# Performance work log

Hardware: AMD Instinct MI355X
Metric: run time of the kernel (lower is better)

## Reference

```python
import jax, jax.numpy as jnp
import numpy as np

DIM = 768
NUM_HEADS = 8
HEAD_DIM = DIM // NUM_HEADS


def setup_inputs() -> dict:
    key = jax.random.key(0)
    k1, k2, k3, k4, k5 = jax.random.split(key, 5)
    B, C, H, W = 16, DIM, 32, 32
    x = jax.random.normal(k1, (B, C, H, W), dtype=jnp.float32)
    # Conv2d 1x1 weights expressed as [out_ch, in_ch] matrices
    w_qkv = jax.random.normal(k2, (3 * C, C), dtype=jnp.float32) * (C ** -0.5)
    b_qkv = jax.random.normal(k3, (3 * C,), dtype=jnp.float32) * 0.02
    w_proj = jax.random.normal(k4, (C, C), dtype=jnp.float32) * (C ** -0.5)
    b_proj = jax.random.normal(k5, (C,), dtype=jnp.float32) * 0.02
    return {"x": x, "w_qkv": w_qkv, "b_qkv": b_qkv, "w_proj": w_proj, "b_proj": b_proj}


def reference(x, w_qkv, b_qkv, w_proj, b_proj):
    B, C, H, W = x.shape
    N = H * W
    nh, hd = NUM_HEADS, C // NUM_HEADS
    xf = x.astype(jnp.float32).reshape(B, C, N)  # bcn
    # 1x1 conv == channel matmul
    qkv = jnp.einsum('oc,bcn->bon', w_qkv, xf) + b_qkv[None, :, None]
    qkv = qkv.reshape(B, 3, nh, hd, N)
    q, k, v = qkv[:, 0], qkv[:, 1], qkv[:, 2]  # [B, nh, hd, N]
    s = hd ** -0.25  # scale split between q and k as in the original
    attn = jnp.einsum('bhdn,bhdm->bhnm', q * s, k * s)  # [B, nh, N, N]
    attn = attn - jax.lax.stop_gradient(jnp.max(attn, axis=-1, keepdims=True))
    attn = jnp.clip(attn, -88.0, 88.0)
    attn = jax.nn.softmax(attn, axis=-1)
    # dropout is identity in eval mode
    out = jnp.einsum('bhnm,bhdm->bhdn', attn, v)  # [B, nh, hd, N]
    out = out.reshape(B, C, N)
    out = jnp.einsum('oc,bcn->bon', w_proj, out) + b_proj[None, :, None]
    return out.reshape(B, C, H, W).astype(x.dtype)
```

## Files before the change

### kernel.cpp

```cpp
#include <hip/hip_runtime.h>
#include <stdint.h>

typedef __attribute__((ext_vector_type(4))) float f32x4;
typedef __attribute__((ext_vector_type(16))) float f32x16;
typedef __attribute__((ext_vector_type(8))) short bf16x8;

#define SQKV 0.38372606f

__device__ __forceinline__ unsigned short f2bf(float f) {
  union { float f; unsigned u; } v; v.f = f;
  unsigned r = v.u + 0x7FFFu + ((v.u >> 16) & 1u);
  return (unsigned short)(r >> 16);
}

__device__ __forceinline__ unsigned cvt_pk_bf16(float a, float b) {
  unsigned r;
  asm volatile("v_cvt_pk_bf16_f32 %0, %1, %2" : "=v"(r) : "v"(a), "v"(b));
  return r;
}
__device__ __forceinline__ void permswap(unsigned &a, unsigned &b) {
  asm volatile("v_permlane32_swap_b32 %0, %1" : "+v"(a), "+v"(b));
}

__device__ __forceinline__ void glds16(const unsigned short* g, unsigned short* l) {
  __builtin_amdgcn_global_load_lds(
      (const __attribute__((address_space(1))) void*)g,
      (__attribute__((address_space(3))) void*)l, 16, 0, 0);
}

__global__ __launch_bounds__(256) void k_convert(const float* __restrict__ src,
                                                 unsigned short* __restrict__ dst,
                                                 int n4) {
  int i = blockIdx.x * 256 + threadIdx.x;
  if (i >= n4) return;
  float4 v = reinterpret_cast<const float4*>(src)[i];
  ushort4 o;
  o.x = f2bf(v.x); o.y = f2bf(v.y); o.z = f2bf(v.z); o.w = f2bf(v.w);
  reinterpret_cast<ushort4*>(dst)[i] = o;
}

__global__ __launch_bounds__(256) void k_transpose(const float* __restrict__ x,
                                                   unsigned short* __restrict__ xT) {
  __shared__ float tile[32][33];
  const int t = threadIdx.x;
  const int j = t & 31, i0 = t >> 5;
  const int n0 = blockIdx.x * 32, c0 = blockIdx.y * 32, b = blockIdx.z;
  const float* src = x + ((size_t)b * 768 + c0) * 1024 + n0;
#pragma unroll
  for (int q = 0; q < 4; ++q)
    tile[i0 + q * 8][j] = src[(size_t)(i0 + q * 8) * 1024 + j];
  __syncthreads();
  unsigned short* dst = xT + ((size_t)b * 1024 + n0) * 768 + c0;
#pragma unroll
  for (int q = 0; q < 4; ++q)
    dst[(size_t)(i0 + q * 8) * 768 + j] = f2bf(tile[j][i0 + q * 8]);
}

__global__ __launch_bounds__(256, 4) void k_gemm_qkv(
    const unsigned short* __restrict__ A,
    const unsigned short* __restrict__ Bx,
    const float* __restrict__ bias,
    unsigned short* __restrict__ qT,
    unsigned short* __restrict__ kT,
    unsigned short* __restrict__ vO) {
  __shared__ unsigned short As[128 * 32];
  __shared__ unsigned short Bs[128 * 32];
  const int t = threadIdx.x;
  const int b = blockIdx.y;
  const int tm = blockIdx.x >> 3, tn = blockIdx.x & 7;
  const int lane = t & 63, w = t >> 6, wr = w >> 1, wc = w & 1;

  const int srow = 16 * w + (lane >> 2);
  const int scol = (lane & 3) << 3;
  const unsigned short* aptr0 = A + (size_t)(tm * 128 + srow) * 768 + scol;
  const unsigned short* aptr1 = aptr0 + (size_t)64 * 768;
  const unsigned short* bptr0 = Bx + (size_t)b * 1024 * 768 + (size_t)(tn * 128 + srow) * 768 + scol;
  const unsigned short* bptr1 = bptr0 + (size_t)64 * 768;
  unsigned short* const lA0 = As + 512 * w;
  unsigned short* const lA1 = As + 2048 + 512 * w;
  unsigned short* const lB0 = Bs + 512 * w;
  unsigned short* const lB1 = Bs + 2048 + 512 * w;

  f32x4 acc[4][4];
#pragma unroll
  for (int mi = 0; mi < 4; ++mi)
#pragma unroll
    for (int ni = 0; ni < 4; ++ni) acc[mi][ni] = (f32x4)0.0f;

  const unsigned short* rA[4];
  const unsigned short* rB[4];
#pragma unroll
  for (int mi = 0; mi < 4; ++mi)
    rA[mi] = As + (wr * 64 + mi * 16 + (lane & 15)) * 32 + ((lane >> 4) << 3);
#pragma unroll
  for (int ni = 0; ni < 4; ++ni)
    rB[ni] = Bs + (wc * 64 + ni * 16 + (lane & 15)) * 32 + ((lane >> 4) << 3);

  for (int kt = 0; kt < 24; ++kt) {
    __syncthreads();
    glds16(aptr0, lA0);
    glds16(aptr1, lA1);
    glds16(bptr0, lB0);
    glds16(bptr1, lB1);
    aptr0 += 32; aptr1 += 32; bptr0 += 32; bptr1 += 32;
    __syncthreads();

    bf16x8 af[4], bfr[4];
#pragma unroll
    for (int mi = 0; mi < 4; ++mi) af[mi] = *reinterpret_cast<const bf16x8*>(rA[mi]);
#pragma unroll
    for (int ni = 0; ni < 4; ++ni) bfr[ni] = *reinterpret_cast<const bf16x8*>(rB[ni]);
#pragma unroll
    for (int mi = 0; mi < 4; ++mi)
#pragma unroll
      for (int ni = 0; ni < 4; ++ni)
        acc[mi][ni] = __builtin_amdgcn_mfma_f32_16x16x32_bf16(af[mi], bfr[ni], acc[mi][ni], 0, 0, 0);
  }

#pragma unroll
  for (int mi = 0; mi < 4; ++mi) {
    const int o0 = tm * 128 + wr * 64 + mi * 16 + ((lane >> 4) << 2);
    const float4 bb = *reinterpret_cast<const float4*>(bias + o0);
    const float sc = (o0 < 1536) ? SQKV : 1.0f;
    const int om = o0 % 768;
    const int hh = om / 96;
    const int d0 = om % 96;
    const int region = o0 / 768;
    const size_t bh = (size_t)(b * 8 + hh);
#pragma unroll
    for (int ni = 0; ni < 4; ++ni) {
      const int nn = tn * 128 + wc * 64 + ni * 16 + (lane & 15);
      ushort4 st;
      st.x = f2bf((acc[mi][ni][0] + bb.x) * sc);
      st.y = f2bf((acc[mi][ni][1] + bb.y) * sc);
      st.z = f2bf((acc[mi][ni][2] + bb.z) * sc);
      st.w = f2bf((acc[mi][ni][3] + bb.w) * sc);
      if (region == 0) {
        *reinterpret_cast<ushort4*>(qT + (bh * 1024 + nn) * 96 + d0) = st;
      } else if (region == 1) {
        *reinterpret_cast<ushort4*>(kT + (bh * 1024 + nn) * 96 + d0) = st;
      } else {
        unsigned short* vp = vO + (bh * 96 + d0) * 1024 + nn;
        vp[0] = st.x; vp[1024] = st.y; vp[2048] = st.z; vp[3072] = st.w;
      }
    }
  }
}

__global__ __launch_bounds__(512, 2) void k_attn2(
    const unsigned short* __restrict__ qT,
    const unsigned short* __restrict__ kT,
    const unsigned short* __restrict__ vO,
    unsigned short* __restrict__ attoutT) {
  __shared__ unsigned short Ks[2][64 * 104];
  __shared__ unsigned short Vs[2][96 * 72];
  __shared__ float redbuf[8][32];

  const int t = threadIdx.x, lane = t & 63, wv = t >> 6;
  const int r31 = lane & 31, h = lane >> 5;
  const int sw = (blockIdx.x & 7) * 64 + (blockIdx.x >> 3);
  const int bh = sw >> 2, qt = sw & 3;
  const int b = bh >> 3, hh = bh & 7;
  const int n0 = qt * 256 + wv * 32;

  bf16x8 Qf[6];
  {
    const unsigned short* qrow = qT + ((size_t)bh * 1024 + n0 + r31) * 96 + h * 8;
#pragma unroll
    for (int ks = 0; ks < 6; ++ks)
      Qf[ks] = *reinterpret_cast<const bf16x8*>(qrow + ks * 16);
  }

  const unsigned short* gptr[3];
  unsigned short* lptr[3];
  int gstep[3], lstride[3];
#pragma unroll
  for (int i = 0; i < 3; ++i) {
    const int cc = t + i * 512;
    if (cc < 768) {
      const int row = cc / 12, col = (cc % 12) * 8;
      gptr[i] = kT + ((size_t)bh * 1024 + row) * 96 + col;
      lptr[i] = &Ks[0][row * 104 + col];
      gstep[i] = 64 * 96;
      lstride[i] = 64 * 104;
    } else {
      const int cv = cc - 768;
      const int d = cv >> 3, col = (cv & 7) * 8;
      gptr[i] = vO + ((size_t)bh * 96 + d) * 1024 + col;
      lptr[i] = &Vs[0][d * 72 + col];
      gstep[i] = 64;
      lstride[i] = 96 * 72;
    }
  }
  uint4 rg[3];
#pragma unroll
  for (int i = 0; i < 3; ++i) rg[i] = *reinterpret_cast<const uint4*>(gptr[i]);

  f32x16 oac[3];
#pragma unroll
  for (int dt = 0; dt < 3; ++dt) oac[dt] = (f32x16)0.0f;
  float run_m = -3.0e38f, run_l = 0.0f;

  int cur = 0;
  for (int mt = 0; mt < 16; ++mt, cur ^= 1) {
#pragma unroll
    for (int i = 0; i < 3; ++i)
      *reinterpret_cast<uint4*>(lptr[i] + cur * lstride[i]) = rg[i];
    __syncthreads();
    if (mt < 15) {
#pragma unroll
      for (int i = 0; i < 3; ++i) {
        gptr[i] += gstep[i];
        rg[i] = *reinterpret_cast<const uint4*>(gptr[i]);
      }
    }
    const unsigned short* Kb = &Ks[cur][0];
    const unsigned short* Vb = &Vs[cur][0];

    f32x16 sa = (f32x16)0.0f, sb = (f32x16)0.0f;
    __builtin_amdgcn_s_setprio(1);
#pragma unroll
    for (int ks = 0; ks < 6; ++ks) {
      const bf16x8 k0 = *reinterpret_cast<const bf16x8*>(Kb + r31 * 104 + ks * 16 + h * 8);
      const bf16x8 k1 = *reinterpret_cast<const bf16x8*>(Kb + (32 + r31) * 104 + ks * 16 + h * 8);
      sa = __builtin_amdgcn_mfma_f32_32x32x16_bf16(k0, Qf[ks], sa, 0, 0, 0);
      sb = __builtin_amdgcn_mfma_f32_32x32x16_bf16(k1, Qf[ks], sb, 0, 0, 0);
    }
    __builtin_amdgcn_s_setprio(0);

    float m4a = fmaxf(sa[0], sa[1]), m4b = fmaxf(sa[2], sa[3]);
    float m4c = fmaxf(sb[0], sb[1]), m4d = fmaxf(sb[2], sb[3]);
#pragma unroll
    for (int i = 4; i < 16; i += 4) {
      m4a = fmaxf(m4a, fmaxf(sa[i], sa[i + 1]));
      m4b = fmaxf(m4b, fmaxf(sa[i + 2], sa[i + 3]));
      m4c = fmaxf(m4c, fmaxf(sb[i], sb[i + 1]));
      m4d = fmaxf(m4d, fmaxf(sb[i + 2], sb[i + 3]));
    }
    float tmax = fmaxf(fmaxf(m4a, m4b), fmaxf(m4c, m4d));
    tmax = fmaxf(tmax, __shfl_xor(tmax, 32));

    if (__any(tmax - run_m > 8.0f)) {
      const float nm = fmaxf(run_m, tmax);
      const float alpha = __builtin_amdgcn_exp2f(run_m - nm);
      run_m = nm;
      run_l *= alpha;
      if (lane < 32) redbuf[wv][lane] = alpha;
      f32x4 a4[4];
#pragma unroll
      for (int q = 0; q < 4; ++q)
        a4[q] = *reinterpret_cast<const f32x4*>(&redbuf[wv][q * 8 + h * 4]);
#pragma unroll
      for (int dt = 0; dt < 3; ++dt)
#pragma unroll
        for (int q = 0; q < 4; ++q)
#pragma unroll
          for (int j = 0; j < 4; ++j)
            oac[dt][q * 4 + j] *= a4[q][j];
    }

    float t0 = 0.f, t1 = 0.f, t2 = 0.f, t3 = 0.f;
#pragma unroll
    for (int i = 0; i < 16; i += 4) {
      sa[i]     = __builtin_amdgcn_exp2f(sa[i] - run_m);     t0 += sa[i];
      sa[i + 1] = __builtin_amdgcn_exp2f(sa[i + 1] - run_m); t1 += sa[i + 1];
      sa[i + 2] = __builtin_amdgcn_exp2f(sa[i + 2] - run_m); t2 += sa[i + 2];
      sa[i + 3] = __builtin_amdgcn_exp2f(sa[i + 3] - run_m); t3 += sa[i + 3];
    }
#pragma unroll
    for (int i = 0; i < 16; i += 4) {
      sb[i]     = __builtin_amdgcn_exp2f(sb[i] - run_m);     t0 += sb[i];
      sb[i + 1] = __builtin_amdgcn_exp2f(sb[i + 1] - run_m); t1 += sb[i + 1];
      sb[i + 2] = __builtin_amdgcn_exp2f(sb[i + 2] - run_m); t2 += sb[i + 2];
      sb[i + 3] = __builtin_amdgcn_exp2f(sb[i + 3] - run_m); t3 += sb[i + 3];
    }
    float ts = (t0 + t1) + (t2 + t3);
    ts += __shfl_xor(ts, 32);
    run_l += ts;

    union { bf16x8 v; unsigned u[4]; } pf;
    __builtin_amdgcn_s_setprio(1);
#pragma unroll
    for (int kst = 0; kst < 4; ++kst) {
      const f32x16& s = (kst < 2) ? sa : sb;
      const int base = (kst & 1) * 8;
      unsigned X = cvt_pk_bf16(s[base + 0], s[base + 1]);
      unsigned Y = cvt_pk_bf16(s[base + 2], s[base + 3]);
      unsigned Z = cvt_pk_bf16(s[base + 4], s[base + 5]);
      unsigned W = cvt_pk_bf16(s[base + 6], s[base + 7]);
      permswap(X, Z);
      permswap(Y, W);
      pf.u[0] = X; pf.u[1] = Y; pf.u[2] = Z; pf.u[3] = W;
#pragma unroll
      for (int dt = 0; dt < 3; ++dt) {
        const bf16x8 vf = *reinterpret_cast<const bf16x8*>(
            Vb + (dt * 32 + r31) * 72 + kst * 16 + h * 8);
        oac[dt] = __builtin_amdgcn_mfma_f32_32x32x16_bf16(pf.v, vf, oac[dt], 0, 0, 0);
      }
    }
    __builtin_amdgcn_s_setprio(0);
  }

  if (lane < 32) redbuf[wv][lane] = 1.0f / run_l;
  f32x4 i4[4];
#pragma unroll
  for (int q = 0; q < 4; ++q)
    i4[q] = *reinterpret_cast<const f32x4*>(&redbuf[wv][q * 8 + h * 4]);
  unsigned short* obase = attoutT + ((size_t)b * 1024 + n0) * 768 + hh * 96;
#pragma unroll
  for (int dt = 0; dt < 3; ++dt)
#pragma unroll
    for (int q = 0; q < 4; ++q)
#pragma unroll
      for (int j = 0; j < 4; ++j) {
        const int np = q * 8 + h * 4 + j;
        obase[(size_t)np * 768 + dt * 32 + r31] = f2bf(oac[dt][q * 4 + j] * i4[q][j]);
      }
}

__global__ __launch_bounds__(256, 4) void k_gemm_proj(
    const unsigned short* __restrict__ Aat,
    const unsigned short* __restrict__ Bw,
    const float* __restrict__ bias,
    float* __restrict__ out) {
  __shared__ unsigned short As[128 * 32];
  __shared__ unsigned short Bs[128 * 32];
  const int t = threadIdx.x;
  const int b = blockIdx.y;
  const int tm = blockIdx.x / 6, tn = blockIdx.x % 6;
  const int lane = t & 63, w = t >> 6, wr = w >> 1, wc = w & 1;

  const int srow = 16 * w + (lane >> 2);
  const int scol = (lane & 3) << 3;
  const unsigned short* aptr0 = Aat + (size_t)b * 1024 * 768 + (size_t)(tm * 128 + srow) * 768 + scol;
  const unsigned short* aptr1 = aptr0 + (size_t)64 * 768;
  const unsigned short* bptr0 = Bw + (size_t)(tn * 128 + srow) * 768 + scol;
  const unsigned short* bptr1 = bptr0 + (size_t)64 * 768;
  unsigned short* const lA0 = As + 512 * w;
  unsigned short* const lA1 = As + 2048 + 512 * w;
  unsigned short* const lB0 = Bs + 512 * w;
  unsigned short* const lB1 = Bs + 2048 + 512 * w;

  f32x4 acc[4][4];
#pragma unroll
  for (int mi = 0; mi < 4; ++mi)
#pragma unroll
    for (int ni = 0; ni < 4; ++ni) acc[mi][ni] = (f32x4)0.0f;

  const unsigned short* rA[4];
  const unsigned short* rB[4];
#pragma unroll
  for (int mi = 0; mi < 4; ++mi)
    rA[mi] = As + (wr * 64 + mi * 16 + (lane & 15)) * 32 + ((lane >> 4) << 3);
#pragma unroll
  for (int ni = 0; ni < 4; ++ni)
    rB[ni] = Bs + (wc * 64 + ni * 16 + (lane & 15)) * 32 + ((lane >> 4) << 3);

  for (int kt = 0; kt < 24; ++kt) {
    __syncthreads();
    glds16(aptr0, lA0);
    glds16(aptr1, lA1);
    glds16(bptr0, lB0);
    glds16(bptr1, lB1);
    aptr0 += 32; aptr1 += 32; bptr0 += 32; bptr1 += 32;
    __syncthreads();

    bf16x8 af[4], bfr[4];
#pragma unroll
    for (int mi = 0; mi < 4; ++mi) af[mi] = *reinterpret_cast<const bf16x8*>(rA[mi]);
#pragma unroll
    for (int ni = 0; ni < 4; ++ni) bfr[ni] = *reinterpret_cast<const bf16x8*>(rB[ni]);
#pragma unroll
    for (int mi = 0; mi < 4; ++mi)
#pragma unroll
      for (int ni = 0; ni < 4; ++ni)
        acc[mi][ni] = __builtin_amdgcn_mfma_f32_16x16x32_bf16(af[mi], bfr[ni], acc[mi][ni], 0, 0, 0);
  }

#pragma unroll
  for (int mi = 0; mi < 4; ++mi) {
    const int n0 = tm * 128 + wr * 64 + mi * 16 + ((lane >> 4) << 2);
#pragma unroll
    for (int ni = 0; ni < 4; ++ni) {
      const int o = tn * 128 + wc * 64 + ni * 16 + (lane & 15);
      const float bo = bias[o];
      float4 vv;
      vv.x = acc[mi][ni][0] + bo;
      vv.y = acc[mi][ni][1] + bo;
      vv.z = acc[mi][ni][2] + bo;
      vv.w = acc[mi][ni][3] + bo;
      *reinterpret_cast<float4*>(out + ((size_t)b * 768 + o) * 1024 + n0) = vv;
    }
  }
}

extern "C" void kernel_launch(void* const* d_in, const int* in_sizes, int n_in,
                              void* d_out, int out_size, void* d_ws, size_t ws_size,
                              hipStream_t stream) {
  const float* x = (const float*)d_in[0];
  const float* w_qkv = (const float*)d_in[1];
  const float* b_qkv = (const float*)d_in[2];
  const float* w_proj = (const float*)d_in[3];
  const float* b_proj = (const float*)d_in[4];
  float* out = (float*)d_out;

  unsigned short* ws = (unsigned short*)d_ws;
  unsigned short* wqkv_bf = ws;
  unsigned short* wproj_bf = wqkv_bf + 2304 * 768;
  unsigned short* xT = wproj_bf + 768 * 768;
  unsigned short* qT = xT + (size_t)16 * 1024 * 768;
  unsigned short* kT = qT + (size_t)16 * 8 * 1024 * 96;
  unsigned short* vO = kT + (size_t)16 * 8 * 1024 * 96;
  unsigned short* attoutT = xT;

  k_convert<<<(2304 * 768 / 4 + 255) / 256, 256, 0, stream>>>(w_qkv, wqkv_bf, 2304 * 768 / 4);
  k_convert<<<(768 * 768 / 4 + 255) / 256, 256, 0, stream>>>(w_proj, wproj_bf, 768 * 768 / 4);
  k_transpose<<<dim3(32, 24, 16), 256, 0, stream>>>(x, xT);
  k_gemm_qkv<<<dim3(144, 16), 256, 0, stream>>>(wqkv_bf, xT, b_qkv, qT, kT, vO);
  k_attn2<<<512, 512, 0, stream>>>(qT, kT, vO, attoutT);
  k_gemm_proj<<<dim3(48, 16), 256, 0, stream>>>(attoutT, wproj_bf, b_proj, out);
}
```

Before: 242.7 us.

## Split softmax into two half-tiles and stagger KV tile order across blocks

The online softmax is now done per 32-key half-tile: the max, rescale and exp for the first half feed its PV MFMAs before the second half is processed, so exp work can overlap with matrix ops. Separately, odd blocks start the KV loop at tile 8 and wrap around, spreading concurrent blocks across different memory regions. The setprio around the PV MFMAs is removed. Rescale checks now run twice per tile, which may trigger more accumulator rescales.

```diff
diff --git a/kernel.cpp b/kernel.cpp
--- a/kernel.cpp
+++ b/kernel.cpp
@@ -162,6 +162,7 @@
   const int bh = sw >> 2, qt = sw & 3;
   const int b = bh >> 3, hh = bh & 7;
   const int n0 = qt * 256 + wv * 32;
+  const int off = (blockIdx.x & 1) * 8;
 
   bf16x8 Qf[6];
   {
@@ -171,7 +172,7 @@
       Qf[ks] = *reinterpret_cast<const bf16x8*>(qrow + ks * 16);
   }
 
-  const unsigned short* gptr[3];
+  const unsigned short* base0[3];
   unsigned short* lptr[3];
   int gstep[3], lstride[3];
 #pragma unroll
@@ -179,14 +180,14 @@
     const int cc = t + i * 512;
     if (cc < 768) {
       const int row = cc / 12, col = (cc % 12) * 8;
-      gptr[i] = kT + ((size_t)bh * 1024 + row) * 96 + col;
+      base0[i] = kT + ((size_t)bh * 1024 + row) * 96 + col;
       lptr[i] = &Ks[0][row * 104 + col];
       gstep[i] = 64 * 96;
       lstride[i] = 64 * 104;
     } else {
       const int cv = cc - 768;
       const int d = cv >> 3, col = (cv & 7) * 8;
-      gptr[i] = vO + ((size_t)bh * 96 + d) * 1024 + col;
+      base0[i] = vO + ((size_t)bh * 96 + d) * 1024 + col;
       lptr[i] = &Vs[0][d * 72 + col];
       gstep[i] = 64;
       lstride[i] = 96 * 72;
@@ -194,7 +195,8 @@
   }
   uint4 rg[3];
 #pragma unroll
-  for (int i = 0; i < 3; ++i) rg[i] = *reinterpret_cast<const uint4*>(gptr[i]);
+  for (int i = 0; i < 3; ++i)
+    rg[i] = *reinterpret_cast<const uint4*>(base0[i] + (size_t)off * gstep[i]);
 
   f32x16 oac[3];
 #pragma unroll
@@ -202,17 +204,16 @@
   float run_m = -3.0e38f, run_l = 0.0f;
 
   int cur = 0;
-  for (int mt = 0; mt < 16; ++mt, cur ^= 1) {
+  for (int it = 0; it < 16; ++it, cur ^= 1) {
 #pragma unroll
     for (int i = 0; i < 3; ++i)
       *reinterpret_cast<uint4*>(lptr[i] + cur * lstride[i]) = rg[i];
     __syncthreads();
-    if (mt < 15) {
-#pragma unroll
-      for (int i = 0; i < 3; ++i) {
-        gptr[i] += gstep[i];
-        rg[i] = *reinterpret_cast<const uint4*>(gptr[i]);
-      }
+    if (it < 15) {
+      const int mtn = (it + 1 + off) & 15;
+#pragma unroll
+      for (int i = 0; i < 3; ++i)
+        rg[i] = *reinterpret_cast<const uint4*>(base0[i] + (size_t)mtn * gstep[i]);
     }
     const unsigned short* Kb = &Ks[cur][0];
     const unsigned short* Vb = &Vs[cur][0];
@@ -228,66 +229,53 @@
     }
     __builtin_amdgcn_s_setprio(0);
 
-    float m4a = fmaxf(sa[0], sa[1]), m4b = fmaxf(sa[2], sa[3]);
-    float m4c = fmaxf(sb[0], sb[1]), m4d = fmaxf(sb[2], sb[3]);
-#pragma unroll
-    for (int i = 4; i < 16; i += 4) {
-      m4a = fmaxf(m4a, fmaxf(sa[i], sa[i + 1]));
-      m4b = fmaxf(m4b, fmaxf(sa[i + 2], sa[i + 3]));
-      m4c = fmaxf(m4c, fmaxf(sb[i], sb[i + 1]));
-      m4d = fmaxf(m4d, fmaxf(sb[i + 2], sb[i + 3]));
-    }
-    float tmax = fmaxf(fmaxf(m4a, m4b), fmaxf(m4c, m4d));
-    tmax = fmaxf(tmax, __shfl_xor(tmax, 32));
-
-    if (__any(tmax - run_m > 8.0f)) {
-      const float nm = fmaxf(run_m, tmax);
-      const float alpha = __builtin_amdgcn_exp2f(run_m - nm);
-      run_m = nm;
-      run_l *= alpha;
-      if (lane < 32) redbuf[wv][lane] = alpha;
-      f32x4 a4[4];
-#pragma unroll
-      for (int q = 0; q < 4; ++q)
-        a4[q] = *reinterpret_cast<const f32x4*>(&redbuf[wv][q * 8 + h * 4]);
-#pragma unroll
-      for (int dt = 0; dt < 3; ++dt)
+    union { bf16x8 v; unsigned u[4]; } pf;
+
+    {
+      float m0 = fmaxf(sa[0], sa[1]), m1 = fmaxf(sa[2], sa[3]);
+      float m2 = fmaxf(sa[4], sa[5]), m3 = fmaxf(sa[6], sa[7]);
+      m0 = fmaxf(m0, fmaxf(sa[8], sa[9]));
+      m1 = fmaxf(m1, fmaxf(sa[10], sa[11]));
+      m2 = fmaxf(m2, fmaxf(sa[12], sa[13]));
+      m3 = fmaxf(m3, fmaxf(sa[14], sa[15]));
+      float tmax = fmaxf(fmaxf(m0, m1), fmaxf(m2, m3));
+      tmax = fmaxf(tmax, __shfl_xor(tmax, 32));
+      if (__any(tmax - run_m > 8.0f)) {
+        const float nm = fmaxf(run_m, tmax);
+        const float alpha = __builtin_amdgcn_exp2f(run_m - nm);
+        run_m = nm; run_l *= alpha;
+        if (lane < 32) redbuf[wv][lane] = alpha;
+        f32x4 a4[4];
 #pragma unroll
         for (int q = 0; q < 4; ++q)
-#pragma unroll
-          for (int j = 0; j < 4; ++j)
-            oac[dt][q * 4 + j] *= a4[q][j];
-    }
-
-    float t0 = 0.f, t1 = 0.f, t2 = 0.f, t3 = 0.f;
-#pragma unroll
-    for (int i = 0; i < 16; i += 4) {
-      sa[i]     = __builtin_amdgcn_exp2f(sa[i] - run_m);     t0 += sa[i];
-      sa[i + 1] = __builtin_amdgcn_exp2f(sa[i + 1] - run_m); t1 += sa[i + 1];
-      sa[i + 2] = __builtin_amdgcn_exp2f(sa[i + 2] - run_m); t2 += sa[i + 2];
-      sa[i + 3] = __builtin_amdgcn_exp2f(sa[i + 3] - run_m); t3 += sa[i + 3];
-    }
-#pragma unroll
-    for (int i = 0; i < 16; i += 4) {
-      sb[i]     = __builtin_amdgcn_exp2f(sb[i] - run_m);     t0 += sb[i];
-      sb[i + 1] = __builtin_amdgcn_exp2f(sb[i + 1] - run_m); t1 += sb[i + 1];
-      sb[i + 2] = __builtin_amdgcn_exp2f(sb[i + 2] - run_m); t2 += sb[i + 2];
-      sb[i + 3] = __builtin_amdgcn_exp2f(sb[i + 3] - run_m); t3 += sb[i + 3];
-    }
-    float ts = (t0 + t1) + (t2 + t3);
-    ts += __shfl_xor(ts, 32);
-    run_l += ts;
-
-    union { bf16x8 v; unsigned u[4]; } pf;
-    __builtin_amdgcn_s_setprio(1);
-#pragma unroll
-    for (int kst = 0; kst < 4; ++kst) {
-      const f32x16& s = (kst < 2) ? sa : sb;
-      const int base = (kst & 1) * 8;
-      unsigned X = cvt_pk_bf16(s[base + 0], s[base + 1]);
-      unsigned Y = cvt_pk_bf16(s[base + 2], s[base + 3]);
-      unsigned Z = cvt_pk_bf16(s[base + 4], s[base + 5]);
-      unsigned W = cvt_pk_bf16(s[base + 6], s[base + 7]);
+          a4[q] = *reinterpret_cast<const f32x4*>(&redbuf[wv][q * 8 + h * 4]);
+#pragma unroll
+        for (int dt = 0; dt < 3; ++dt)
+#pragma unroll
+          for (int q = 0; q < 4; ++q)
+#pragma unroll
+            for (int j = 0; j < 4; ++j)
+              oac[dt][q * 4 + j] *= a4[q][j];
+      }
+      float t0 = 0.f, t1 = 0.f, t2 = 0.f, t3 = 0.f;
+#pragma unroll
+      for (int i = 0; i < 16; i += 4) {
+        sa[i]     = __builtin_amdgcn_exp2f(sa[i] - run_m);     t0 += sa[i];
+        sa[i + 1] = __builtin_amdgcn_exp2f(sa[i + 1] - run_m); t1 += sa[i + 1];
+        sa[i + 2] = __builtin_amdgcn_exp2f(sa[i + 2] - run_m); t2 += sa[i + 2];
+        sa[i + 3] = __builtin_amdgcn_exp2f(sa[i + 3] - run_m); t3 += sa[i + 3];
+      }
+      float ts = (t0 + t1) + (t2 + t3);
+      ts += __shfl_xor(ts, 32);
+      run_l += ts;
+    }
+#pragma unroll
+    for (int kst = 0; kst < 2; ++kst) {
+      const int base = kst * 8;
+      unsigned X = cvt_pk_bf16(sa[base + 0], sa[base + 1]);
+      unsigned Y = cvt_pk_bf16(sa[base + 2], sa[base + 3]);
+      unsigned Z = cvt_pk_bf16(sa[base + 4], sa[base + 5]);
+      unsigned W = cvt_pk_bf16(sa[base + 6], sa[base + 7]);
       permswap(X, Z);
       permswap(Y, W);
       pf.u[0] = X; pf.u[1] = Y; pf.u[2] = Z; pf.u[3] = W;
@@ -298,7 +286,62 @@
         oac[dt] = __builtin_amdgcn_mfma_f32_32x32x16_bf16(pf.v, vf, oac[dt], 0, 0, 0);
       }
     }
-    __builtin_amdgcn_s_setprio(0);
+
+    {
+      float m0 = fmaxf(sb[0], sb[1]), m1 = fmaxf(sb[2], sb[3]);
+      float m2 = fmaxf(sb[4], sb[5]), m3 = fmaxf(sb[6], sb[7]);
+      m0 = fmaxf(m0, fmaxf(sb[8], sb[9]));
+      m1 = fmaxf(m1, fmaxf(sb[10], sb[11]));
+      m2 = fmaxf(m2, fmaxf(sb[12], sb[13]));
+      m3 = fmaxf(m3, fmaxf(sb[14], sb[15]));
+      float tmax = fmaxf(fmaxf(m0, m1), fmaxf(m2, m3));
+      tmax = fmaxf(tmax, __shfl_xor(tmax, 32));
+      if (__any(tmax - run_m > 8.0f)) {
+        const float nm = fmaxf(run_m, tmax);
+        const float alpha = __builtin_amdgcn_exp2f(run_m - nm);
+        run_m = nm; run_l *= alpha;
+        if (lane < 32) redbuf[wv][lane] = alpha;
+        f32x4 a4[4];
+#pragma unroll
+        for (int q = 0; q < 4; ++q)
+          a4[q] = *reinterpret_cast<const f32x4*>(&redbuf[wv][q * 8 + h * 4]);
+#pragma unroll
+        for (int dt = 0; dt < 3; ++dt)
+#pragma unroll
+          for (int q = 0; q < 4; ++q)
+#pragma unroll
+            for (int j = 0; j < 4; ++j)
+              oac[dt][q * 4 + j] *= a4[q][j];
+      }
+      float t0 = 0.f, t1 = 0.f, t2 = 0.f, t3 = 0.f;
+#pragma unroll
+      for (int i = 0; i < 16; i += 4) {
+        sb[i]     = __builtin_amdgcn_exp2f(sb[i] - run_m);     t0 += sb[i];
+        sb[i + 1] = __builtin_amdgcn_exp2f(sb[i + 1] - run_m); t1 += sb[i + 1];
+        sb[i + 2] = __builtin_amdgcn_exp2f(sb[i + 2] - run_m); t2 += sb[i + 2];
+        sb[i + 3] = __builtin_amdgcn_exp2f(sb[i + 3] - run_m); t3 += sb[i + 3];
+      }
+      float ts = (t0 + t1) + (t2 + t3);
+      ts += __shfl_xor(ts, 32);
+      run_l += ts;
+    }
+#pragma unroll
+    for (int kst = 2; kst < 4; ++kst) {
+      const int base = (kst & 1) * 8;
+      unsigned X = cvt_pk_bf16(sb[base + 0], sb[base + 1]);
+      unsigned Y = cvt_pk_bf16(sb[base + 2], sb[base + 3]);
+      unsigned Z = cvt_pk_bf16(sb[base + 4], sb[base + 5]);
+      unsigned W = cvt_pk_bf16(sb[base + 6], sb[base + 7]);
+      permswap(X, Z);
+      permswap(Y, W);
+      pf.u[0] = X; pf.u[1] = Y; pf.u[2] = Z; pf.u[3] = W;
+#pragma unroll
+      for (int dt = 0; dt < 3; ++dt) {
+        const bf16x8 vf = *reinterpret_cast<const bf16x8*>(
+            Vb + (dt * 32 + r31) * 72 + kst * 16 + h * 8);
+        oac[dt] = __builtin_amdgcn_mfma_f32_32x32x16_bf16(pf.v, vf, oac[dt], 0, 0, 0);
+      }
+    }
   }
 
   if (lane < 32) redbuf[wv][lane] = 1.0f / run_l;
```

New measurement: 244.5 us. About the same (+0.7%).
